# Kernel optimization log

Hardware: AMD Instinct MI355X
Metric: run time of the kernel (lower is better)

Reference implementation:

```python
import jax, jax.numpy as jnp
import numpy as np

B, L, D = 2, 2048, 1024
H = 16
HD = D // H  # 64


def _orthogonal_projection(key, d, m):
    g = jax.random.normal(key, (d, m), dtype=jnp.float32)
    q, r = jnp.linalg.qr(g)
    s = jnp.sign(jnp.diagonal(r))
    s = jnp.where(s == 0, 1.0, s)
    q = q * s[None, :]
    # preserve_variance=True
    return q * np.sqrt(d / m)


def setup_inputs() -> dict:
    key = jax.random.key(0)
    ks = jax.random.split(key, 8)
    x = jax.random.normal(ks[0], (B, L, D), dtype=jnp.float32)
    p = jax.random.normal(ks[1], (B, L, D), dtype=jnp.float32)
    s = 1.0 / np.sqrt(D)
    W_qkv = jax.random.uniform(ks[2], (3 * D, D), dtype=jnp.float32, minval=-s, maxval=s)
    b_qkv = jax.random.uniform(ks[3], (3 * D,), dtype=jnp.float32, minval=-s, maxval=s)
    W_out = jax.random.uniform(ks[4], (D, D), dtype=jnp.float32, minval=-s, maxval=s)
    b_out = jax.random.uniform(ks[5], (D,), dtype=jnp.float32, minval=-s, maxval=s)
    proj = _orthogonal_projection(ks[6], D, D // 2)
    return {"x": x, "p": p, "W_qkv": W_qkv, "b_qkv": b_qkv,
            "W_out": W_out, "b_out": b_out, "proj": proj}


def reference(x, p, W_qkv, b_qkv, W_out, b_out, proj):
    # QKV projection: (B,L,D) -> (B,L,3,H,HD)
    qkv = (jnp.einsum('bld,ed->ble', x, W_qkv) + b_qkv).reshape(B, L, 3, H, HD)
    q, k, v = qkv[:, :, 0], qkv[:, :, 1], qkv[:, :, 2]

    # Collaborative rotary phases from conditioning tokens: (B,L,H,HD/2)
    phases = (p @ proj).reshape(B, L, H, HD // 2)  # phase_scale = 1.0
    cos, sin = jnp.cos(phases), jnp.sin(phases)

    half = HD // 2
    # non-interleaved rotary: split head_dim into two halves
    def rot(t):
        t1, t2 = t[..., :half], t[..., half:]
        return jnp.concatenate([t1 * cos - t2 * sin, t1 * sin + t2 * cos], axis=-1)

    q, k = rot(q), rot(k)

    scale = HD ** -0.5
    scores = jnp.einsum('bqhd,bkhd->bhqk', q, k) * scale
    attn = jax.nn.softmax(scores, axis=-1)
    out = jnp.einsum('bhqk,bkhd->bqhd', attn, v).reshape(B, L, D)
    return jnp.einsum('bld,ed->ble', out, W_out) + b_out
```

## Files before the change

### kernel.cpp

```cpp
#include <hip/hip_runtime.h>
#include <hip/hip_bf16.h>
#include <math.h>

namespace {
constexpr int Bb = 2;
constexpr int Ll = 2048;
constexpr int Dd = 1024;
constexpr int Hh = 16;
constexpr int NT = Bb * Ll;
constexpr int D3 = 3 * Dd;
constexpr int PH = Dd / 2;
constexpr int LDK = 72;
}

typedef __attribute__((ext_vector_type(8))) short bf16x8;
typedef __attribute__((ext_vector_type(4))) short bf16x4;
typedef __attribute__((ext_vector_type(4))) float f32x4;

#if defined(__has_builtin)
#if __has_builtin(__builtin_amdgcn_mfma_f32_16x16x16bf16_1k)
#define HAVE_MFMA16 1
#endif
#endif

__device__ inline unsigned pack2bf(float a, float b) {
  __hip_bfloat162 t = __float22bfloat162_rn(float2{a, b});
  union { __hip_bfloat162 h; unsigned u; } cv; cv.h = t;
  return cv.u;
}

__device__ inline bf16x4 u2bf4(uint2 u) {
  union { uint2 u; bf16x4 v; } c; c.u = u; return c.v;
}

__device__ inline float bfhalf(unsigned u, int hi) {
  union { unsigned u; float f; } c;
  c.u = hi ? (u & 0xffff0000u) : (u << 16);
  return c.f;
}

__device__ inline f32x4 pv_mfma(bf16x4 va, bf16x4 vb, f32x4 c) {
#ifdef HAVE_MFMA16
  return __builtin_amdgcn_mfma_f32_16x16x16bf16_1k(va, vb, c, 0, 0, 0);
#else
  const bf16x8 a8 = {va[0], va[1], va[2], va[3], 0, 0, 0, 0};
  const bf16x8 b8 = {vb[0], vb[1], vb[2], vb[3], 0, 0, 0, 0};
  return __builtin_amdgcn_mfma_f32_16x16x32_bf16(a8, b8, c, 0, 0, 0);
#endif
}

__device__ inline void async_cp16(const void* gsrc, void* ldst) {
  __builtin_amdgcn_global_load_lds(
      (const __attribute__((address_space(1))) unsigned int*)gsrc,
      (__attribute__((address_space(3))) unsigned int*)ldst, 16, 0, 0);
}

__global__ __launch_bounds__(256) void prep_kernel(
    const float4* __restrict__ p, uint2* __restrict__ p_hi4, uint2* __restrict__ p_lo4,
    const float* __restrict__ proj, short* __restrict__ th, short* __restrict__ tl,
    const float4* __restrict__ x, const float4* __restrict__ wq, const float4* __restrict__ wo,
    uint2* __restrict__ xd, uint2* __restrict__ wqd, uint2* __restrict__ wod)
{
  __shared__ float Ls[64][65];
  const int bid = blockIdx.x;
  const int tid = threadIdx.x;

  if (bid < 4096) {
    const int i = bid * 256 + tid;
    const float4 f = p[i];
    float hf[4], lf[4];
    const float ff[4] = {f.x, f.y, f.z, f.w};
#pragma unroll
    for (int j = 0; j < 4; ++j) {
      const __hip_bfloat16 h = __float2bfloat16(ff[j]);
      hf[j] = __bfloat162float(h);
      lf[j] = ff[j] - hf[j];
    }
    p_hi4[i] = make_uint2(pack2bf(hf[0], hf[1]), pack2bf(hf[2], hf[3]));
    p_lo4[i] = make_uint2(pack2bf(lf[0], lf[1]), pack2bf(lf[2], lf[3]));
  } else if (bid < 4224) {
    const int bx = bid - 4096;
    const int d0 = (bx & 15) * 64, m0 = (bx >> 4) * 64;
    const int r = tid >> 4, c4 = (tid & 15) * 4;
#pragma unroll
    for (int it = 0; it < 4; ++it) {
      const int row = it * 16 + r;
      const float4 v = *(const float4*)&proj[(size_t)(d0 + row) * PH + m0 + c4];
      Ls[row][c4] = v.x; Ls[row][c4+1] = v.y; Ls[row][c4+2] = v.z; Ls[row][c4+3] = v.w;
    }
    __syncthreads();
#pragma unroll
    for (int it = 0; it < 4; ++it) {
      const int row = it * 16 + r;
      float hf[4], lf[4];
#pragma unroll
      for (int j = 0; j < 4; ++j) {
        const float v = Ls[c4 + j][row];
        const __hip_bfloat16 h = __float2bfloat16(v);
        hf[j] = __bfloat162float(h);
        lf[j] = v - hf[j];
      }
      *(uint2*)&th[(size_t)(m0 + row) * Dd + d0 + c4] = make_uint2(pack2bf(hf[0], hf[1]), pack2bf(hf[2], hf[3]));
      *(uint2*)&tl[(size_t)(m0 + row) * Dd + d0 + c4] = make_uint2(pack2bf(lf[0], lf[1]), pack2bf(lf[2], lf[3]));
    }
  } else {
    int i = (bid - 4224) * 256 + tid;
    const float4* s; uint2* d;
    if (i < 1048576) { s = x; d = xd; }
    else if (i < 1048576 + 786432) { i -= 1048576; s = wq; d = wqd; }
    else { i -= 1048576 + 786432; s = wo; d = wod; }
    const float4 f = s[i];
    d[i] = make_uint2(pack2bf(f.x, f.y), pack2bf(f.z, f.w));
  }
}

__global__ __launch_bounds__(256) void gemm_nn_split(
    const short* __restrict__ Ah_g, const short* __restrict__ Al_g,
    const short* __restrict__ Wh_g, const short* __restrict__ Wl_g,
    float* __restrict__ C)
{
  __shared__ __align__(16) short Ah[128 * 32], Al[128 * 32], Wh[64 * 32], Wl[64 * 32];
  const int tid = threadIdx.x;
  const int w = tid >> 6, lane = tid & 63;
  const int l15 = lane & 15, quad = lane >> 4;
  const int n0 = blockIdx.y * 128, m0 = blockIdx.x * 64;

  const int row = tid >> 2, cc = tid & 3;
  const int ksw = (cc ^ (row & 3)) * 8;
  const short* gAh = Ah_g + (size_t)(n0 + row) * Dd + ksw;
  const short* gAl = Al_g + (size_t)(n0 + row) * Dd + ksw;
  const short* gWh = Wh_g + (size_t)(m0 + row) * Dd + ksw;
  const short* gWl = Wl_g + (size_t)(m0 + row) * Dd + ksw;
  short* lAh  = Ah + tid * 8;
  short* lAh2 = Ah + 2048 + tid * 8;
  short* lAl  = Al + tid * 8;
  short* lAl2 = Al + 2048 + tid * 8;
  short* lWh  = Wh + tid * 8;
  short* lWl  = Wl + tid * 8;

  f32x4 acc[2][4];
#pragma unroll
  for (int i = 0; i < 2; ++i)
#pragma unroll
    for (int j = 0; j < 4; ++j) acc[i][j] = f32x4{0.f, 0.f, 0.f, 0.f};

  const int swq = (quad ^ (l15 & 3)) * 8;

  for (int k0 = 0; k0 < Dd; k0 += 32) {
    __syncthreads();
    async_cp16(gAh + k0, lAh);
    async_cp16(gAh + 64 * Dd + k0, lAh2);
    async_cp16(gAl + k0, lAl);
    async_cp16(gAl + 64 * Dd + k0, lAl2);
    async_cp16(gWh + k0, lWh);
    async_cp16(gWl + k0, lWl);
    __syncthreads();

    bf16x8 ah[2], al[2], wh[4], wl[4];
#pragma unroll
    for (int i = 0; i < 2; ++i) {
      ah[i] = *(const bf16x8*)&Ah[(w * 32 + i * 16 + l15) * 32 + swq];
      al[i] = *(const bf16x8*)&Al[(w * 32 + i * 16 + l15) * 32 + swq];
    }
#pragma unroll
    for (int j = 0; j < 4; ++j) {
      wh[j] = *(const bf16x8*)&Wh[(j * 16 + l15) * 32 + swq];
      wl[j] = *(const bf16x8*)&Wl[(j * 16 + l15) * 32 + swq];
    }
#pragma unroll
    for (int i = 0; i < 2; ++i)
#pragma unroll
      for (int j = 0; j < 4; ++j) {
        acc[i][j] = __builtin_amdgcn_mfma_f32_16x16x32_bf16(ah[i], wh[j], acc[i][j], 0, 0, 0);
        acc[i][j] = __builtin_amdgcn_mfma_f32_16x16x32_bf16(ah[i], wl[j], acc[i][j], 0, 0, 0);
        acc[i][j] = __builtin_amdgcn_mfma_f32_16x16x32_bf16(al[i], wh[j], acc[i][j], 0, 0, 0);
      }
  }

#pragma unroll
  for (int i = 0; i < 2; ++i)
#pragma unroll
    for (int r = 0; r < 4; ++r) {
      float* crow = C + (size_t)(n0 + w * 32 + i * 16 + quad * 4 + r) * PH + m0 + l15;
#pragma unroll
      for (int j = 0; j < 4; ++j) crow[j * 16] = acc[i][j][r];
    }
}

__global__ __launch_bounds__(256) void gemm_qkv_fused(
    const __hip_bfloat16* __restrict__ A, const __hip_bfloat16* __restrict__ W,
    const float* __restrict__ bias, const float* __restrict__ phases,
    __hip_bfloat16* __restrict__ q_bf, __hip_bfloat16* __restrict__ k_bf,
    __hip_bfloat16* __restrict__ vt_g)
{
  __shared__ __align__(16) short As[128 * 32];
  __shared__ __align__(16) short Ws[128 * 32];
  const int tid = threadIdx.x;
  const int w = tid >> 6, lane = tid & 63;
  const int l15 = lane & 15, quad = lane >> 4;
  const int wn = w >> 1, wm = w & 1;
  const int n0 = blockIdx.y * 128, m0 = blockIdx.x * 128;

  const int row = tid >> 2, cc = tid & 3;
  const int ksw = (cc ^ (row & 3)) * 8;
  const short* gA  = (const short*)A + (size_t)(n0 + row) * Dd + ksw;
  const short* gW  = (const short*)W + (size_t)(m0 + row) * Dd + ksw;
  short* lA  = As + tid * 8;
  short* lA2 = As + 2048 + tid * 8;
  short* lW  = Ws + tid * 8;
  short* lW2 = Ws + 2048 + tid * 8;

  f32x4 acc[4][4];
#pragma unroll
  for (int i = 0; i < 4; ++i)
#pragma unroll
    for (int j = 0; j < 4; ++j) acc[i][j] = f32x4{0.f, 0.f, 0.f, 0.f};

  const int swq = (quad ^ (l15 & 3)) * 8;

  for (int k0 = 0; k0 < Dd; k0 += 32) {
    __syncthreads();
    async_cp16(gA + k0, lA);
    async_cp16(gA + 64 * Dd + k0, lA2);
    async_cp16(gW + k0, lW);
    async_cp16(gW + 64 * Dd + k0, lW2);
    __syncthreads();

    bf16x8 af[4], bf[4];
#pragma unroll
    for (int i = 0; i < 4; ++i)
      af[i] = *(const bf16x8*)&As[(wn * 64 + i * 16 + l15) * 32 + swq];
#pragma unroll
    for (int j = 0; j < 4; ++j)
      bf[j] = *(const bf16x8*)&Ws[(wm * 64 + j * 16 + l15) * 32 + swq];
#pragma unroll
    for (int i = 0; i < 4; ++i)
#pragma unroll
      for (int j = 0; j < 4; ++j)
        acc[i][j] = __builtin_amdgcn_mfma_f32_16x16x32_bf16(af[i], bf[j], acc[i][j], 0, 0, 0);
  }

  float bv[4];
#pragma unroll
  for (int j = 0; j < 4; ++j) bv[j] = bias[m0 + wm * 64 + j * 16 + l15];

  const int region = m0 >> 10;
  const int mloc = (m0 & 1023) + wm * 64;
  const int h = mloc >> 6;

  if (region < 2) {
    __hip_bfloat16* dst = region == 0 ? q_bf : k_bf;
    const float SC = region == 0 ? 0.18033688011112042f : 1.0f;
#pragma unroll
    for (int i = 0; i < 4; ++i)
#pragma unroll
      for (int r = 0; r < 4; ++r) {
        const int n = n0 + wn * 64 + i * 16 + quad * 4 + r;
        const float* phrow = phases + (size_t)n * PH + h * 32;
        __hip_bfloat16* drow = dst + (size_t)n * Dd + h * 64;
#pragma unroll
        for (int pz = 0; pz < 2; ++pz) {
          const float ph = phrow[pz * 16 + l15];
          float sn, cs;
          __sincosf(ph, &sn, &cs);
          const float a1 = acc[i][pz][r] + bv[pz];
          const float a2 = acc[i][pz + 2][r] + bv[pz + 2];
          drow[pz * 16 + l15]      = __float2bfloat16((a1 * cs - a2 * sn) * SC);
          drow[pz * 16 + 32 + l15] = __float2bfloat16((a1 * sn + a2 * cs) * SC);
        }
      }
  } else {
    const int bh = (n0 >> 11) * 16 + h;
    const int tokb = (n0 & 2047) + wn * 64;
#pragma unroll
    for (int i = 0; i < 4; ++i)
#pragma unroll
      for (int j = 0; j < 4; ++j) {
        const uint2 o = make_uint2(
            pack2bf(acc[i][j][0] + bv[j], acc[i][j][1] + bv[j]),
            pack2bf(acc[i][j][2] + bv[j], acc[i][j][3] + bv[j]));
        const int d = j * 16 + l15;
        *(uint2*)&vt_g[(size_t)(bh * 64 + d) * Ll + tokb + i * 16 + quad * 4] = o;
      }
  }
}

__global__ __launch_bounds__(256) void gemm_bt_64(
    const __hip_bfloat16* __restrict__ A, const __hip_bfloat16* __restrict__ W,
    const float* __restrict__ bias, float* __restrict__ C, int K, int M)
{
  __shared__ __align__(16) short As[128 * 32];
  __shared__ __align__(16) short Ws[64 * 32];
  const int tid = threadIdx.x;
  const int w = tid >> 6, lane = tid & 63;
  const int l15 = lane & 15, quad = lane >> 4;
  const int n0 = blockIdx.y * 128, m0 = blockIdx.x * 64;

  const int row = tid >> 2, cc = tid & 3;
  const int ksw = (cc ^ (row & 3)) * 8;
  const short* gA = (const short*)A + (size_t)(n0 + row) * K + ksw;
  const short* gW = (const short*)W + (size_t)(m0 + row) * K + ksw;
  short* lA  = As + tid * 8;
  short* lA2 = As + 2048 + tid * 8;
  short* lW  = Ws + tid * 8;

  f32x4 acc[2][4];
#pragma unroll
  for (int i = 0; i < 2; ++i)
#pragma unroll
    for (int j = 0; j < 4; ++j) acc[i][j] = f32x4{0.f, 0.f, 0.f, 0.f};

  const int swq = (quad ^ (l15 & 3)) * 8;

  for (int k0 = 0; k0 < K; k0 += 32) {
    __syncthreads();
    async_cp16(gA + k0, lA);
    async_cp16(gA + 64 * K + k0, lA2);
    async_cp16(gW + k0, lW);
    __syncthreads();

    bf16x8 af[2], bf[4];
#pragma unroll
    for (int i = 0; i < 2; ++i)
      af[i] = *(const bf16x8*)&As[(w * 32 + i * 16 + l15) * 32 + swq];
#pragma unroll
    for (int j = 0; j < 4; ++j)
      bf[j] = *(const bf16x8*)&Ws[(j * 16 + l15) * 32 + swq];
#pragma unroll
    for (int i = 0; i < 2; ++i)
#pragma unroll
      for (int j = 0; j < 4; ++j)
        acc[i][j] = __builtin_amdgcn_mfma_f32_16x16x32_bf16(af[i], bf[j], acc[i][j], 0, 0, 0);
  }

  float bv[4];
#pragma unroll
  for (int j = 0; j < 4; ++j) bv[j] = bias[m0 + j * 16 + l15];
#pragma unroll
  for (int i = 0; i < 2; ++i)
#pragma unroll
    for (int r = 0; r < 4; ++r) {
      float* crow = C + (size_t)(n0 + w * 32 + i * 16 + quad * 4 + r) * M + m0 + l15;
#pragma unroll
      for (int j = 0; j < 4; ++j) crow[j * 16] = acc[i][j][r] + bv[j];
    }
}

__global__ __launch_bounds__(256) void attn_mfma(
    const __hip_bfloat16* __restrict__ q_bf,
    const __hip_bfloat16* __restrict__ k_bf,
    const __hip_bfloat16* __restrict__ vt_g,
    __hip_bfloat16* __restrict__ o_part,
    float* __restrict__ lden_g)
{
  __shared__ __align__(16) short Ks[64 * LDK];
  __shared__ __align__(16) short Vt[64 * LDK];

  const int tid = threadIdx.x;
  const int w = tid >> 6;
  const int lane = tid & 63;
  const int l15 = lane & 15;
  const int quad = lane >> 4;

  const int q0 = blockIdx.x * 128;
  const int bh = blockIdx.y;
  const int kz = blockIdx.z;
  const int b = bh >> 4, h = bh & 15;
  const int kt0 = kz * 16;

  bf16x8 qfrag[2][2];
#pragma unroll
  for (int qg = 0; qg < 2; ++qg)
#pragma unroll
    for (int kh = 0; kh < 2; ++kh) {
      const size_t qrow = (size_t)(b * Ll + q0 + w * 32 + qg * 16 + l15);
      qfrag[qg][kh] = *(const bf16x8*)(q_bf + qrow * Dd + h * 64 + kh * 32 + quad * 8);
    }

  f32x4 acc[4][2];
#pragma unroll
  for (int dt = 0; dt < 4; ++dt)
#pragma unroll
    for (int qg = 0; qg < 2; ++qg) acc[dt][qg] = f32x4{0.f, 0.f, 0.f, 0.f};
  f32x4 lden[2] = {f32x4{0.f,0.f,0.f,0.f}, f32x4{0.f,0.f,0.f,0.f}};
  const short one_bf = (short)0x3F80;
  const bf16x4 ones = {one_bf, one_bf, one_bf, one_bf};

  const int srow = tid >> 2, sseg = tid & 3;
  const __hip_bfloat16* kbase = k_bf + (size_t)(b * Ll + srow) * Dd + h * 64 + sseg * 16;
  const __hip_bfloat16* vbase = vt_g + ((size_t)(bh * 64 + srow)) * Ll + sseg * 16;

  uint4 pk0, pk1, pv0, pv1;
  {
    const uint4* kg = (const uint4*)(kbase + (size_t)kt0 * 64 * Dd);
    pk0 = kg[0]; pk1 = kg[1];
    const uint4* vg = (const uint4*)(vbase + kt0 * 64);
    pv0 = vg[0]; pv1 = vg[1];
  }

  for (int kt = 0; kt < 16; ++kt) {
    __syncthreads();
    *(uint4*)&Ks[srow * LDK + sseg * 16]     = pk0;
    *(uint4*)&Ks[srow * LDK + sseg * 16 + 8] = pk1;
    *(uint4*)&Vt[srow * LDK + sseg * 16]     = pv0;
    *(uint4*)&Vt[srow * LDK + sseg * 16 + 8] = pv1;
    __syncthreads();

    {
      const int ktn = kt0 + ((kt + 1) & 15);
      const uint4* kg = (const uint4*)(kbase + (size_t)ktn * 64 * Dd);
      pk0 = kg[0]; pk1 = kg[1];
      const uint4* vg = (const uint4*)(vbase + ktn * 64);
      pv0 = vg[0]; pv1 = vg[1];
    }

    f32x4 s[4][2];
#pragma unroll
    for (int n = 0; n < 4; ++n)
#pragma unroll
      for (int qg = 0; qg < 2; ++qg) s[n][qg] = f32x4{0.f, 0.f, 0.f, 0.f};
#pragma unroll
    for (int n = 0; n < 4; ++n)
#pragma unroll
      for (int kh = 0; kh < 2; ++kh) {
        const bf16x8 af = *(const bf16x8*)&Ks[(n * 16 + l15) * LDK + kh * 32 + quad * 8];
        s[n][0] = __builtin_amdgcn_mfma_f32_16x16x32_bf16(af, qfrag[0][kh], s[n][0], 0, 0, 0);
        s[n][1] = __builtin_amdgcn_mfma_f32_16x16x32_bf16(af, qfrag[1][kh], s[n][1], 0, 0, 0);
      }

    uint2 bq[4][2];
#pragma unroll
    for (int qg = 0; qg < 2; ++qg)
#pragma unroll
      for (int n = 0; n < 4; ++n) {
        union { float f; unsigned u; } p0, p1, p2, p3;
        p0.f = __builtin_amdgcn_exp2f(s[n][qg][0]);
        p1.f = __builtin_amdgcn_exp2f(s[n][qg][1]);
        p2.f = __builtin_amdgcn_exp2f(s[n][qg][2]);
        p3.f = __builtin_amdgcn_exp2f(s[n][qg][3]);
        bq[n][qg] = make_uint2(__builtin_amdgcn_perm(p1.u, p0.u, 0x07060302u),
                               __builtin_amdgcn_perm(p3.u, p2.u, 0x07060302u));
      }

#pragma unroll
    for (int n = 0; n < 4; ++n) {
      const bf16x4 pb0 = u2bf4(bq[n][0]);
      const bf16x4 pb1 = u2bf4(bq[n][1]);
      lden[0] = pv_mfma(ones, pb0, lden[0]);
      lden[1] = pv_mfma(ones, pb1, lden[1]);
#pragma unroll
      for (int dt = 0; dt < 4; ++dt) {
        const bf16x4 va = *(const bf16x4*)&Vt[(dt * 16 + l15) * LDK + n * 16 + quad * 4];
        acc[dt][0] = pv_mfma(va, pb0, acc[dt][0]);
        acc[dt][1] = pv_mfma(va, pb1, acc[dt][1]);
      }
    }
  }

#pragma unroll
  for (int qg = 0; qg < 2; ++qg) {
    const float lv = lden[qg][0];
    const float linv = 1.f / lv;
    const int ql = q0 + w * 32 + qg * 16 + l15;
    if (quad == 0)
      lden_g[((size_t)(kz * Bb + b) * Hh + h) * Ll + ql] = lv;
    __hip_bfloat16* dst = o_part + ((size_t)kz * NT + b * Ll + ql) * Dd + h * 64;
#pragma unroll
    for (int dt = 0; dt < 4; ++dt) {
      const uint2 o = make_uint2(
          pack2bf(acc[dt][qg][0] * linv, acc[dt][qg][1] * linv),
          pack2bf(acc[dt][qg][2] * linv, acc[dt][qg][3] * linv));
      *(uint2*)&dst[dt * 16 + quad * 4] = o;
    }
  }
}

__global__ __launch_bounds__(256) void attn_combine(
    const __hip_bfloat16* __restrict__ o_part, const float* __restrict__ lden_g,
    __hip_bfloat16* __restrict__ aout)
{
  const int i = blockIdx.x * 256 + threadIdx.x;
  const int n = i >> 8, d4 = i & 255;
  const int b = n >> 11, l = n & 2047;
  const int h = d4 >> 4;
  const float l0 = lden_g[((size_t)b * Hh + h) * Ll + l];
  const float l1 = lden_g[((size_t)(Bb + b) * Hh + h) * Ll + l];
  const float inv = 1.f / (l0 + l1);
  const float w0 = l0 * inv, w1 = l1 * inv;
  const uint2 a0 = ((const uint2*)o_part)[i];
  const uint2 a1 = ((const uint2*)o_part)[(NT * (size_t)Dd / 4) + i];
  const float r0 = w0 * bfhalf(a0.x, 0) + w1 * bfhalf(a1.x, 0);
  const float r1 = w0 * bfhalf(a0.x, 1) + w1 * bfhalf(a1.x, 1);
  const float r2 = w0 * bfhalf(a0.y, 0) + w1 * bfhalf(a1.y, 0);
  const float r3 = w0 * bfhalf(a0.y, 1) + w1 * bfhalf(a1.y, 1);
  ((uint2*)aout)[i] = make_uint2(pack2bf(r0, r1), pack2bf(r2, r3));
}

extern "C" void kernel_launch(void* const* d_in, const int* in_sizes, int n_in,
                              void* d_out, int out_size, void* d_ws, size_t ws_size,
                              hipStream_t stream) {
  const float* x     = (const float*)d_in[0];
  const float* p     = (const float*)d_in[1];
  const float* W_qkv = (const float*)d_in[2];
  const float* b_qkv = (const float*)d_in[3];
  const float* W_out = (const float*)d_in[4];
  const float* b_out = (const float*)d_in[5];
  const float* proj  = (const float*)d_in[6];
  float* out = (float*)d_out;

  char* wsb = (char*)d_ws;
  float*          phases   = (float*)(wsb);
  short*          p_hi     = (short*)(wsb + (8u << 20));
  __hip_bfloat16* aout_bf  = (__hip_bfloat16*)(wsb + (8u << 20));
  short*          p_lo     = (short*)(wsb + (16u << 20));
  __hip_bfloat16* vt_g     = (__hip_bfloat16*)(wsb + (16u << 20));
  short*          projt_hi = (short*)(wsb + (24u << 20));
  short*          projt_lo = (short*)(wsb + (25u << 20));
  __hip_bfloat16* q_bf     = (__hip_bfloat16*)(wsb + (26u << 20));
  __hip_bfloat16* k_bf     = (__hip_bfloat16*)(wsb + (34u << 20));
  __hip_bfloat16* x_bf     = (__hip_bfloat16*)(wsb + (42u << 20));
  __hip_bfloat16* o_part   = (__hip_bfloat16*)(wsb + (42u << 20));
  __hip_bfloat16* wqkv_bf  = (__hip_bfloat16*)(wsb + (50u << 20));
  __hip_bfloat16* wout_bf  = (__hip_bfloat16*)(wsb + (58u << 20));
  float*          lden_g   = (float*)(wsb + (60u << 20));

  prep_kernel<<<12416, 256, 0, stream>>>(
      (const float4*)p, (uint2*)p_hi, (uint2*)p_lo,
      proj, projt_hi, projt_lo,
      (const float4*)x, (const float4*)W_qkv, (const float4*)W_out,
      (uint2*)x_bf, (uint2*)wqkv_bf, (uint2*)wout_bf);
  gemm_nn_split<<<dim3(PH / 64, NT / 128), 256, 0, stream>>>(p_hi, p_lo, projt_hi, projt_lo, phases);
  gemm_qkv_fused<<<dim3(D3 / 128, NT / 128), 256, 0, stream>>>(x_bf, wqkv_bf, b_qkv, phases,
                                                               q_bf, k_bf, vt_g);
  attn_mfma<<<dim3(Ll / 128, Bb * Hh, 2), 256, 0, stream>>>(q_bf, k_bf, vt_g, o_part, lden_g);
  attn_combine<<<4096, 256, 0, stream>>>(o_part, lden_g, aout_bf);
  gemm_bt_64<<<dim3(Dd / 64, NT / 128), 256, 0, stream>>>(aout_bf, wout_bf, b_out, out, Dd, Dd);
}
```

Measured before the change: 262.5 us.

## Use K=32 MFMA for PV via permlane swaps; shrink phase GEMM tile

```diff
diff --git a/kernel.cpp b/kernel.cpp
--- a/kernel.cpp
+++ b/kernel.cpp
@@ -14,14 +14,7 @@
 }
 
 typedef __attribute__((ext_vector_type(8))) short bf16x8;
-typedef __attribute__((ext_vector_type(4))) short bf16x4;
 typedef __attribute__((ext_vector_type(4))) float f32x4;
-
-#if defined(__has_builtin)
-#if __has_builtin(__builtin_amdgcn_mfma_f32_16x16x16bf16_1k)
-#define HAVE_MFMA16 1
-#endif
-#endif
 
 __device__ inline unsigned pack2bf(float a, float b) {
   __hip_bfloat162 t = __float22bfloat162_rn(float2{a, b});
@@ -29,24 +22,10 @@
   return cv.u;
 }
 
-__device__ inline bf16x4 u2bf4(uint2 u) {
-  union { uint2 u; bf16x4 v; } c; c.u = u; return c.v;
-}
-
 __device__ inline float bfhalf(unsigned u, int hi) {
   union { unsigned u; float f; } c;
   c.u = hi ? (u & 0xffff0000u) : (u << 16);
   return c.f;
-}
-
-__device__ inline f32x4 pv_mfma(bf16x4 va, bf16x4 vb, f32x4 c) {
-#ifdef HAVE_MFMA16
-  return __builtin_amdgcn_mfma_f32_16x16x16bf16_1k(va, vb, c, 0, 0, 0);
-#else
-  const bf16x8 a8 = {va[0], va[1], va[2], va[3], 0, 0, 0, 0};
-  const bf16x8 b8 = {vb[0], vb[1], vb[2], vb[3], 0, 0, 0, 0};
-  return __builtin_amdgcn_mfma_f32_16x16x32_bf16(a8, b8, c, 0, 0, 0);
-#endif
 }
 
 __device__ inline void async_cp16(const void* gsrc, void* ldst) {
@@ -119,11 +98,11 @@
     const short* __restrict__ Wh_g, const short* __restrict__ Wl_g,
     float* __restrict__ C)
 {
-  __shared__ __align__(16) short Ah[128 * 32], Al[128 * 32], Wh[64 * 32], Wl[64 * 32];
+  __shared__ __align__(16) short Ah[64 * 32], Al[64 * 32], Wh[64 * 32], Wl[64 * 32];
   const int tid = threadIdx.x;
   const int w = tid >> 6, lane = tid & 63;
   const int l15 = lane & 15, quad = lane >> 4;
-  const int n0 = blockIdx.y * 128, m0 = blockIdx.x * 64;
+  const int n0 = blockIdx.y * 64, m0 = blockIdx.x * 64;
 
   const int row = tid >> 2, cc = tid & 3;
   const int ksw = (cc ^ (row & 3)) * 8;
@@ -131,60 +110,47 @@
   const short* gAl = Al_g + (size_t)(n0 + row) * Dd + ksw;
   const short* gWh = Wh_g + (size_t)(m0 + row) * Dd + ksw;
   const short* gWl = Wl_g + (size_t)(m0 + row) * Dd + ksw;
-  short* lAh  = Ah + tid * 8;
-  short* lAh2 = Ah + 2048 + tid * 8;
-  short* lAl  = Al + tid * 8;
-  short* lAl2 = Al + 2048 + tid * 8;
-  short* lWh  = Wh + tid * 8;
-  short* lWl  = Wl + tid * 8;
-
-  f32x4 acc[2][4];
-#pragma unroll
-  for (int i = 0; i < 2; ++i)
-#pragma unroll
-    for (int j = 0; j < 4; ++j) acc[i][j] = f32x4{0.f, 0.f, 0.f, 0.f};
+  short* lAh = Ah + tid * 8;
+  short* lAl = Al + tid * 8;
+  short* lWh = Wh + tid * 8;
+  short* lWl = Wl + tid * 8;
+
+  f32x4 acc[4];
+#pragma unroll
+  for (int j = 0; j < 4; ++j) acc[j] = f32x4{0.f, 0.f, 0.f, 0.f};
 
   const int swq = (quad ^ (l15 & 3)) * 8;
 
   for (int k0 = 0; k0 < Dd; k0 += 32) {
     __syncthreads();
     async_cp16(gAh + k0, lAh);
-    async_cp16(gAh + 64 * Dd + k0, lAh2);
     async_cp16(gAl + k0, lAl);
-    async_cp16(gAl + 64 * Dd + k0, lAl2);
     async_cp16(gWh + k0, lWh);
     async_cp16(gWl + k0, lWl);
     __syncthreads();
 
-    bf16x8 ah[2], al[2], wh[4], wl[4];
-#pragma unroll
-    for (int i = 0; i < 2; ++i) {
-      ah[i] = *(const bf16x8*)&Ah[(w * 32 + i * 16 + l15) * 32 + swq];
-      al[i] = *(const bf16x8*)&Al[(w * 32 + i * 16 + l15) * 32 + swq];
-    }
+    bf16x8 ah, al, wh[4], wl[4];
+    ah = *(const bf16x8*)&Ah[(w * 16 + l15) * 32 + swq];
+    al = *(const bf16x8*)&Al[(w * 16 + l15) * 32 + swq];
 #pragma unroll
     for (int j = 0; j < 4; ++j) {
       wh[j] = *(const bf16x8*)&Wh[(j * 16 + l15) * 32 + swq];
       wl[j] = *(const bf16x8*)&Wl[(j * 16 + l15) * 32 + swq];
     }
 #pragma unroll
-    for (int i = 0; i < 2; ++i)
-#pragma unroll
-      for (int j = 0; j < 4; ++j) {
-        acc[i][j] = __builtin_amdgcn_mfma_f32_16x16x32_bf16(ah[i], wh[j], acc[i][j], 0, 0, 0);
-        acc[i][j] = __builtin_amdgcn_mfma_f32_16x16x32_bf16(ah[i], wl[j], acc[i][j], 0, 0, 0);
-        acc[i][j] = __builtin_amdgcn_mfma_f32_16x16x32_bf16(al[i], wh[j], acc[i][j], 0, 0, 0);
-      }
-  }
-
-#pragma unroll
-  for (int i = 0; i < 2; ++i)
-#pragma unroll
-    for (int r = 0; r < 4; ++r) {
-      float* crow = C + (size_t)(n0 + w * 32 + i * 16 + quad * 4 + r) * PH + m0 + l15;
-#pragma unroll
-      for (int j = 0; j < 4; ++j) crow[j * 16] = acc[i][j][r];
-    }
+    for (int j = 0; j < 4; ++j) {
+      acc[j] = __builtin_amdgcn_mfma_f32_16x16x32_bf16(ah, wh[j], acc[j], 0, 0, 0);
+      acc[j] = __builtin_amdgcn_mfma_f32_16x16x32_bf16(ah, wl[j], acc[j], 0, 0, 0);
+      acc[j] = __builtin_amdgcn_mfma_f32_16x16x32_bf16(al, wh[j], acc[j], 0, 0, 0);
+    }
+  }
+
+#pragma unroll
+  for (int r = 0; r < 4; ++r) {
+    float* crow = C + (size_t)(n0 + w * 16 + quad * 4 + r) * PH + m0 + l15;
+#pragma unroll
+    for (int j = 0; j < 4; ++j) crow[j * 16] = acc[j][r];
+  }
 }
 
 __global__ __launch_bounds__(256) void gemm_qkv_fused(
@@ -384,7 +350,7 @@
     for (int qg = 0; qg < 2; ++qg) acc[dt][qg] = f32x4{0.f, 0.f, 0.f, 0.f};
   f32x4 lden[2] = {f32x4{0.f,0.f,0.f,0.f}, f32x4{0.f,0.f,0.f,0.f}};
   const short one_bf = (short)0x3F80;
-  const bf16x4 ones = {one_bf, one_bf, one_bf, one_bf};
+  const bf16x8 ones8 = {one_bf, one_bf, one_bf, one_bf, one_bf, one_bf, one_bf, one_bf};
 
   const int srow = tid >> 2, sseg = tid & 3;
   const __hip_bfloat16* kbase = k_bf + (size_t)(b * Ll + srow) * Dd + h * 64 + sseg * 16;
@@ -443,16 +409,25 @@
       }
 
 #pragma unroll
-    for (int n = 0; n < 4; ++n) {
-      const bf16x4 pb0 = u2bf4(bq[n][0]);
-      const bf16x4 pb1 = u2bf4(bq[n][1]);
-      lden[0] = pv_mfma(ones, pb0, lden[0]);
-      lden[1] = pv_mfma(ones, pb1, lden[1]);
-#pragma unroll
-      for (int dt = 0; dt < 4; ++dt) {
-        const bf16x4 va = *(const bf16x4*)&Vt[(dt * 16 + l15) * LDK + n * 16 + quad * 4];
-        acc[dt][0] = pv_mfma(va, pb0, acc[dt][0]);
-        acc[dt][1] = pv_mfma(va, pb1, acc[dt][1]);
+    for (int pr = 0; pr < 2; ++pr) {
+      bf16x8 va[4];
+#pragma unroll
+      for (int dt = 0; dt < 4; ++dt)
+        va[dt] = *(const bf16x8*)&Vt[(dt * 16 + l15) * LDK + pr * 32 + quad * 8];
+#pragma unroll
+      for (int qg = 0; qg < 2; ++qg) {
+        const uint2 a = bq[2 * pr][qg];
+        const uint2 c = bq[2 * pr + 1][qg];
+        auto rx32 = __builtin_amdgcn_permlane32_swap(a.x, c.x, false, false);
+        auto rx16 = __builtin_amdgcn_permlane16_swap(rx32[0], rx32[1], false, false);
+        auto ry32 = __builtin_amdgcn_permlane32_swap(a.y, c.y, false, false);
+        auto ry16 = __builtin_amdgcn_permlane16_swap(ry32[0], ry32[1], false, false);
+        union { unsigned u[4]; bf16x8 v; } pb;
+        pb.u[0] = rx16[0]; pb.u[1] = ry16[0]; pb.u[2] = rx16[1]; pb.u[3] = ry16[1];
+        lden[qg] = __builtin_amdgcn_mfma_f32_16x16x32_bf16(ones8, pb.v, lden[qg], 0, 0, 0);
+#pragma unroll
+        for (int dt = 0; dt < 4; ++dt)
+          acc[dt][qg] = __builtin_amdgcn_mfma_f32_16x16x32_bf16(va[dt], pb.v, acc[dt][qg], 0, 0, 0);
       }
     }
   }
@@ -529,7 +504,7 @@
       proj, projt_hi, projt_lo,
       (const float4*)x, (const float4*)W_qkv, (const float4*)W_out,
       (uint2*)x_bf, (uint2*)wqkv_bf, (uint2*)wout_bf);
-  gemm_nn_split<<<dim3(PH / 64, NT / 128), 256, 0, stream>>>(p_hi, p_lo, projt_hi, projt_lo, phases);
+  gemm_nn_split<<<dim3(PH / 64, NT / 64), 256, 0, stream>>>(p_hi, p_lo, projt_hi, projt_lo, phases);
   gemm_qkv_fused<<<dim3(D3 / 128, NT / 128), 256, 0, stream>>>(x_bf, wqkv_bf, b_qkv, phases,
                                                                q_bf, k_bf, vt_g);
   attn_mfma<<<dim3(Ll / 128, Bb * Hh, 2), 256, 0, stream>>>(q_bf, k_bf, vt_g, o_part, lden_g);
```

New measurement: 252.7 us. -3.7%, faster.
